# Optimization experiments

Measured on AMD Instinct MI355X. Metric: run time of the kernel, lower is better.

The kernel has to match this reference:

```python
import jax, jax.numpy as jnp
import numpy as np

# torch semantics: m = x > 0; y = x[m]  (flattened stream compaction);
# unsqueeze(0) then squeeze([0]) is an identity.
# JAX/jit cannot return data-dependent shapes, so we return the compacted
# values moved to the front of a fixed-size buffer (padded with 0) plus the
# valid count. y_padded[:count] == torch's y.

def reference(x):
    xf = x.reshape(-1)                      # [N]
    mask = xf > 0.0                         # [N] bool
    count = jnp.sum(mask)                   # scalar int: number of valid elems
    # stable argsort on ~mask moves True-mask positions to the front,
    # preserving original order (matches masked_select ordering)
    order = jnp.argsort(jnp.logical_not(mask), stable=True)  # [N]
    n = xf.shape[0]
    y_padded = jnp.where(jnp.arange(n) < count, xf[order], 0.0)  # [N]
    return y_padded, count


def setup_inputs() -> dict:
    key = jax.random.key(0)
    x = jax.random.normal(key, (64, 1024, 1024), dtype=jnp.float32)
    return {"x": x}
```

## Files before the change

### kernel.cpp

```cpp
#include <hip/hip_runtime.h>


#define BLOCK 256
#define CHUNK 4096
#define SCAN_THREADS 1024
#define SCAN_VPT 16

__global__ void k_count(const float* __restrict__ x, int n, int* __restrict__ blockSums) {
    const int tid = threadIdx.x;
    const int base = blockIdx.x * CHUNK;
    int cnt = 0;
#pragma unroll
    for (int k = 0; k < 4; ++k) {
        const int i = base + k * 1024 + tid * 4;
        if (i + 3 < n) {
            const float4 v = *reinterpret_cast<const float4*>(x + i);
            cnt += (v.x > 0.f) + (v.y > 0.f) + (v.z > 0.f) + (v.w > 0.f);
        } else {
            for (int j = i; j < i + 4 && j < n; ++j) cnt += (x[j] > 0.f);
        }
    }
#pragma unroll
    for (int off = 32; off > 0; off >>= 1) cnt += __shfl_down(cnt, off, 64);
    __shared__ int lds[4];
    if ((tid & 63) == 0) lds[tid >> 6] = cnt;
    __syncthreads();
    if (tid == 0) blockSums[blockIdx.x] = lds[0] + lds[1] + lds[2] + lds[3];
}

__global__ void k_scan(int* __restrict__ sums, int numBlocks,
                       int* __restrict__ countOut, float* __restrict__ countOutF) {
    __shared__ int lds[32];
    const int tid  = threadIdx.x;
    const int lane = tid & 63;
    const int wave = tid >> 6;

    int vals[SCAN_VPT];
    const int base = tid * SCAN_VPT;
    int local = 0;
#pragma unroll
    for (int j = 0; j < SCAN_VPT; ++j) {
        const int i = base + j;
        const int v = (i < numBlocks) ? sums[i] : 0;
        vals[j] = local;
        local += v;
    }
    int incl = local;
#pragma unroll
    for (int off = 1; off < 64; off <<= 1) {
        const int y = __shfl_up(incl, off, 64);
        if (lane >= off) incl += y;
    }
    if (lane == 63) lds[wave] = incl;
    __syncthreads();
    if (wave == 0 && lane < 16) {
        int w = lds[lane];
#pragma unroll
        for (int off = 1; off < 16; off <<= 1) {
            const int y = __shfl_up(w, off, 16);
            if ((lane & 15) >= off) w += y;
        }
        lds[16 + lane] = w;
    }
    __syncthreads();
    const int waveEx   = (wave == 0) ? 0 : lds[16 + wave - 1];
    const int threadEx = waveEx + incl - local;
#pragma unroll
    for (int j = 0; j < SCAN_VPT; ++j) {
        const int i = base + j;
        if (i < numBlocks) sums[i] = threadEx + vals[j];
    }
    if (tid == SCAN_THREADS - 1) {
        const int total = waveEx + incl;
        *countOut  = total;
        *countOutF = (float)total;
    }
}

__device__ __forceinline__ int block_scan_excl_256(int val, int* lds, int* blockTotal) {
    const int tid  = threadIdx.x;
    const int lane = tid & 63;
    const int wave = tid >> 6;
    int incl = val;
#pragma unroll
    for (int off = 1; off < 64; off <<= 1) {
        const int y = __shfl_up(incl, off, 64);
        if (lane >= off) incl += y;
    }
    if (lane == 63) lds[wave] = incl;
    __syncthreads();
    if (tid == 0) {
        const int s0 = lds[0], s1 = lds[1], s2 = lds[2], s3 = lds[3];
        lds[4] = 0; lds[5] = s0; lds[6] = s0 + s1; lds[7] = s0 + s1 + s2;
        lds[8] = s0 + s1 + s2 + s3;
    }
    __syncthreads();
    const int ex = lds[4 + wave] + incl - val;
    *blockTotal = lds[8];
    __syncthreads();
    return ex;
}

__global__ void k_scatter(const float* __restrict__ x, int n,
                          const int* __restrict__ blockOffsets, float* __restrict__ y) {
    __shared__ int lds[9];
    const int tid  = threadIdx.x;
    const int base = blockIdx.x * CHUNK;
    int offset = blockOffsets[blockIdx.x];
#pragma unroll
    for (int k = 0; k < 4; ++k) {
        const int i = base + k * 1024 + tid * 4;
        float a0 = 0.f, a1 = 0.f, a2 = 0.f, a3 = 0.f;
        if (i + 3 < n) {
            const float4 v = *reinterpret_cast<const float4*>(x + i);
            a0 = v.x; a1 = v.y; a2 = v.z; a3 = v.w;
        } else {
            if (i + 0 < n) a0 = x[i + 0];
            if (i + 1 < n) a1 = x[i + 1];
            if (i + 2 < n) a2 = x[i + 2];
            if (i + 3 < n) a3 = x[i + 3];
        }
        const int m0 = a0 > 0.f, m1 = a1 > 0.f, m2 = a2 > 0.f, m3 = a3 > 0.f;
        int total;
        const int rank = block_scan_excl_256(m0 + m1 + m2 + m3, lds, &total);
        int o = offset + rank;
        if (m0) y[o++] = a0;
        if (m1) y[o++] = a1;
        if (m2) y[o++] = a2;
        if (m3) y[o++] = a3;
        offset += total;
    }
}

__global__ void k_zerofill(float* __restrict__ y, const int* __restrict__ count, int n) {
    const int i = (blockIdx.x * BLOCK + threadIdx.x) * 4;
    if (i >= n) return;
    const int c = *count;
    if (i + 4 <= c) return;
    const int start = (i > c) ? i : c;
    const int end   = (i + 4 < n) ? i + 4 : n;
    if (start == i && end == i + 4) {
        *reinterpret_cast<float4*>(y + i) = make_float4(0.f, 0.f, 0.f, 0.f);
    } else {
        for (int j = start; j < end; ++j) y[j] = 0.f;
    }
}

extern "C" void kernel_launch(void* const* d_in, const int* in_sizes, int n_in,
                              void* d_out, int out_size, void* d_ws, size_t ws_size,
                              hipStream_t stream) {
    const float* x = (const float*)d_in[0];
    float* y = (float*)d_out;
    const int n = in_sizes[0];

    int* blockSums = (int*)d_ws;
    const int numBlocks = (n + CHUNK - 1) / CHUNK;
    int* countPtr = blockSums + numBlocks;

    k_count<<<numBlocks, BLOCK, 0, stream>>>(x, n, blockSums);
    k_scan<<<1, SCAN_THREADS, 0, stream>>>(blockSums, numBlocks,
                                           countPtr, y + (out_size - 1));
    k_scatter<<<numBlocks, BLOCK, 0, stream>>>(x, n, blockSums, y);
    const int zfBlocks = ((n + 3) / 4 + BLOCK - 1) / BLOCK;
    k_zerofill<<<zfBlocks, BLOCK, 0, stream>>>(y, countPtr, n);
}
```

Baseline: 519.1 us.

## Stage compacted values in LDS and write them out coalesced per block

The scatter kernel now loads 16 contiguous values per thread and runs a single block scan instead of four. It compacts the positive values into shared memory, then writes them to global memory with contiguous thread-strided stores. The goal is to replace scattered per-thread global writes with coalesced ones and to cut the number of block-wide scans and barriers. In exchange it uses 16KB of LDS per block, which can limit occupancy, and the per-thread strided loads are less coalesced than the previous interleaved layout.

```diff
diff --git a/kernel.cpp b/kernel.cpp
--- a/kernel.cpp
+++ b/kernel.cpp
@@ -2,23 +2,23 @@
 
 
 #define BLOCK 256
-#define CHUNK 4096
+#define VPT 16
+#define CHUNK (BLOCK * VPT)
 #define SCAN_THREADS 1024
 #define SCAN_VPT 16
 
 __global__ void k_count(const float* __restrict__ x, int n, int* __restrict__ blockSums) {
     const int tid = threadIdx.x;
-    const int base = blockIdx.x * CHUNK;
+    const long long tbase = (long long)blockIdx.x * CHUNK + tid * VPT;
     int cnt = 0;
+    if (tbase + VPT <= n) {
 #pragma unroll
-    for (int k = 0; k < 4; ++k) {
-        const int i = base + k * 1024 + tid * 4;
-        if (i + 3 < n) {
-            const float4 v = *reinterpret_cast<const float4*>(x + i);
+        for (int k = 0; k < 4; ++k) {
+            const float4 v = *reinterpret_cast<const float4*>(x + tbase + 4 * k);
             cnt += (v.x > 0.f) + (v.y > 0.f) + (v.z > 0.f) + (v.w > 0.f);
-        } else {
-            for (int j = i; j < i + 4 && j < n; ++j) cnt += (x[j] > 0.f);
         }
+    } else {
+        for (long long j = tbase; j < tbase + VPT && j < n; ++j) cnt += (x[j] > 0.f);
     }
 #pragma unroll
     for (int off = 32; off > 0; off >>= 1) cnt += __shfl_down(cnt, off, 64);
@@ -97,52 +97,59 @@
     __syncthreads();
     const int ex = lds[4 + wave] + incl - val;
     *blockTotal = lds[8];
-    __syncthreads();
     return ex;
 }
 
 __global__ void k_scatter(const float* __restrict__ x, int n,
                           const int* __restrict__ blockOffsets, float* __restrict__ y) {
-    __shared__ int lds[9];
-    const int tid  = threadIdx.x;
-    const int base = blockIdx.x * CHUNK;
-    int offset = blockOffsets[blockIdx.x];
+    __shared__ float vals[CHUNK];
+    __shared__ int scan_lds[9];
+    const int tid = threadIdx.x;
+    const long long tbase = (long long)blockIdx.x * CHUNK + tid * VPT;
+
+    float v[VPT];
+    if (tbase + VPT <= n) {
 #pragma unroll
-    for (int k = 0; k < 4; ++k) {
-        const int i = base + k * 1024 + tid * 4;
-        float a0 = 0.f, a1 = 0.f, a2 = 0.f, a3 = 0.f;
-        if (i + 3 < n) {
-            const float4 v = *reinterpret_cast<const float4*>(x + i);
-            a0 = v.x; a1 = v.y; a2 = v.z; a3 = v.w;
-        } else {
-            if (i + 0 < n) a0 = x[i + 0];
-            if (i + 1 < n) a1 = x[i + 1];
-            if (i + 2 < n) a2 = x[i + 2];
-            if (i + 3 < n) a3 = x[i + 3];
+        for (int k = 0; k < 4; ++k) {
+            const float4 f = *reinterpret_cast<const float4*>(x + tbase + 4 * k);
+            v[4 * k + 0] = f.x; v[4 * k + 1] = f.y; v[4 * k + 2] = f.z; v[4 * k + 3] = f.w;
         }
-        const int m0 = a0 > 0.f, m1 = a1 > 0.f, m2 = a2 > 0.f, m3 = a3 > 0.f;
-        int total;
-        const int rank = block_scan_excl_256(m0 + m1 + m2 + m3, lds, &total);
-        int o = offset + rank;
-        if (m0) y[o++] = a0;
-        if (m1) y[o++] = a1;
-        if (m2) y[o++] = a2;
-        if (m3) y[o++] = a3;
-        offset += total;
+    } else {
+#pragma unroll
+        for (int j = 0; j < VPT; ++j)
+            v[j] = (tbase + j < n) ? x[tbase + j] : 0.f;
+    }
+
+    int c = 0;
+#pragma unroll
+    for (int j = 0; j < VPT; ++j) c += (v[j] > 0.f);
+
+    int total;
+    int r = block_scan_excl_256(c, scan_lds, &total);
+
+#pragma unroll
+    for (int j = 0; j < VPT; ++j) {
+        if (v[j] > 0.f) vals[r++] = v[j];
+    }
+    __syncthreads();
+
+    const int offset = blockOffsets[blockIdx.x];
+    for (int j = tid; j < total; j += BLOCK) {
+        y[offset + j] = vals[j];
     }
 }
 
 __global__ void k_zerofill(float* __restrict__ y, const int* __restrict__ count, int n) {
-    const int i = (blockIdx.x * BLOCK + threadIdx.x) * 4;
+    const long long i = ((long long)blockIdx.x * BLOCK + threadIdx.x) * 4;
     if (i >= n) return;
     const int c = *count;
     if (i + 4 <= c) return;
-    const int start = (i > c) ? i : c;
-    const int end   = (i + 4 < n) ? i + 4 : n;
+    const long long start = (i > c) ? i : c;
+    const long long end   = (i + 4 < n) ? i + 4 : n;
     if (start == i && end == i + 4) {
         *reinterpret_cast<float4*>(y + i) = make_float4(0.f, 0.f, 0.f, 0.f);
     } else {
-        for (int j = start; j < end; ++j) y[j] = 0.f;
+        for (long long j = start; j < end; ++j) y[j] = 0.f;
     }
 }
 
```

Result: faster. 504.4 us (-2.8%).
